# Optimization experiments

Measured on AMD Instinct MI355X. Metric: run time of the kernel, lower is better.

## Reference

```python
import jax, jax.numpy as jnp
import numpy as np

N, E = 50000, 800000
IN, HID, HEADS, OUT = 128, 64, 2, 32
SLOPE = 0.2  # PyG leaky_relu default


def gat_conv(x, edge_index, edge_attr, W, att_src, att_dst, W_edge, att_edge, bias,
             heads, out_ch, concat):
    n = x.shape[0]
    src, dst = edge_index[0], edge_index[1]
    # add_self_loops with fill_value='mean': self-loop attr = mean of incoming edge_attr
    ones = jnp.ones((src.shape[0],), x.dtype)
    deg = jax.ops.segment_sum(ones, dst, num_segments=n)
    loop_attr = jax.ops.segment_sum(edge_attr, dst, num_segments=n) / jnp.maximum(deg, 1.0)[:, None]
    ar = jnp.arange(n)
    src = jnp.concatenate([src, ar])
    dst = jnp.concatenate([dst, ar])
    ea = jnp.concatenate([edge_attr, loop_attr], axis=0)  # [E+N, 1]
    # linear projections
    h = (x @ W).reshape(n, heads, out_ch)                      # [N,H,C]
    a_src = jnp.sum(h * att_src, axis=-1)                      # [N,H]
    a_dst = jnp.sum(h * att_dst, axis=-1)                      # [N,H]
    e_emb = (ea @ W_edge).reshape(-1, heads, out_ch)           # [E+N,H,C]
    a_edge = jnp.sum(e_emb * att_edge, axis=-1)                # [E+N,H]
    alpha = jax.nn.leaky_relu(a_src[src] + a_dst[dst] + a_edge, SLOPE)
    # segment softmax over destination nodes
    amax = jax.ops.segment_max(alpha, dst, num_segments=n)
    amax = jnp.where(jnp.isfinite(amax), amax, 0.0)
    ex = jnp.exp(alpha - amax[dst])
    denom = jax.ops.segment_sum(ex, dst, num_segments=n)
    coef = ex / (denom[dst] + 1e-16)                           # [E+N,H]
    out = jax.ops.segment_sum(h[src] * coef[:, :, None], dst, num_segments=n)  # [N,H,C]
    out = out.reshape(n, heads * out_ch) if concat else out.mean(axis=1)
    return out + bias


def setup_inputs() -> dict:
    key = jax.random.key(0)
    ks = jax.random.split(key, 16)
    g = lambda k, shape, fan: (jax.random.normal(k, shape, jnp.float32) / np.float32(np.sqrt(fan)))
    x = jax.random.normal(ks[0], (N, IN), jnp.float32)
    edge_index = jax.random.randint(ks[1], (2, E), 0, N)
    edge_weight = jax.random.uniform(ks[2], (E, 1), jnp.float32)
    return dict(
        x=x, edge_index=edge_index, edge_weight=edge_weight,
        W1=g(ks[3], (IN, HEADS * HID), IN),
        att_src1=g(ks[4], (1, HEADS, HID), HID),
        att_dst1=g(ks[5], (1, HEADS, HID), HID),
        We1=g(ks[6], (1, HEADS * HID), 1),
        att_edge1=g(ks[7], (1, HEADS, HID), HID),
        b1=jnp.zeros((HEADS * HID,), jnp.float32),
        W2=g(ks[8], (HEADS * HID, OUT), HEADS * HID),
        att_src2=g(ks[9], (1, 1, OUT), OUT),
        att_dst2=g(ks[10], (1, 1, OUT), OUT),
        We2=g(ks[11], (1, OUT), 1),
        att_edge2=g(ks[12], (1, 1, OUT), OUT),
        b2=jnp.zeros((OUT,), jnp.float32),
    )


def reference(x, edge_index, edge_weight, W1, att_src1, att_dst1, We1, att_edge1, b1,
              W2, att_src2, att_dst2, We2, att_edge2, b2):
    h = gat_conv(x, edge_index, edge_weight, W1, att_src1, att_dst1, We1, att_edge1, b1,
                 HEADS, HID, True)
    h = jax.nn.elu(h)
    out = gat_conv(h, edge_index, edge_weight, W2, att_src2, att_dst2, We2, att_edge2, b2,
                   1, OUT, False)
    return out
```

## Files before the change

kernel.cpp:

```cpp
#include <hip/hip_runtime.h>
#include <hip/hip_bf16.h>
#include <hip/hip_fp16.h>
#include <cstddef>

#define NN 50000
#define EE 800000
#define SB  196

typedef _Float16 half4v __attribute__((ext_vector_type(4)));
typedef _Float16 half8v __attribute__((ext_vector_type(8)));
typedef _Float16 h2v    __attribute__((ext_vector_type(2)));
typedef float    f32x4  __attribute__((ext_vector_type(4)));

__global__ void zero_k(unsigned long long* __restrict__ p) {
    int i = blockIdx.x * blockDim.x + threadIdx.x;
    if (i < NN) p[i] = 0ULL;
}

__global__ void hist_k(const int* __restrict__ ei, const float* __restrict__ ew,
                       unsigned long long* __restrict__ packed, int* __restrict__ rank) {
    int e = blockIdx.x * blockDim.x + threadIdx.x;
    if (e >= EE) return;
    int dst = ei[EE + e];
    unsigned q = (unsigned)(ew[e] * 16777216.0f + 0.5f);
    unsigned long long old =
        atomicAdd(&packed[dst], (1ULL << 40) | (unsigned long long)q);
    rank[e] = (int)(old >> 40);
}

__global__ void loopdiv_k(const unsigned long long* __restrict__ packed,
                          int* __restrict__ deg, float* __restrict__ loopa,
                          int* __restrict__ bsum) {
    __shared__ int sm[256];
    int t = threadIdx.x, n = blockIdx.x * 256 + t;
    int d = 0;
    if (n < NN) {
        unsigned long long p = packed[n];
        d = (int)(p >> 40);
        float ls = (float)(p & ((1ULL << 40) - 1)) * (1.0f / 16777216.0f);
        deg[n] = d;
        loopa[n] = ls / fmaxf((float)d, 1.0f);
    }
    sm[t] = d;
    __syncthreads();
    for (int off = 128; off; off >>= 1) {
        if (t < off) sm[t] += sm[t + off];
        __syncthreads();
    }
    if (!t) bsum[blockIdx.x] = sm[0];
}

__global__ void scan_top_k(const int* __restrict__ bsum, int* __restrict__ boff) {
    __shared__ int sm[256];
    int t = threadIdx.x;
    int v = (t < SB) ? bsum[t] : 0;
    sm[t] = v;
    __syncthreads();
    for (int off = 1; off < 256; off <<= 1) {
        int a = (t >= off) ? sm[t - off] : 0;
        __syncthreads();
        sm[t] += a;
        __syncthreads();
    }
    boff[t] = sm[t] - v;
}

__global__ void scan_final_k(const int* __restrict__ deg, const int* __restrict__ boff,
                             int* __restrict__ rowptr) {
    __shared__ int sm[256];
    int t = threadIdx.x, i = blockIdx.x * 256 + t;
    int v = (i < NN) ? deg[i] : 0;
    sm[t] = v;
    __syncthreads();
    for (int off = 1; off < 256; off <<= 1) {
        int a = (t >= off) ? sm[t - off] : 0;
        __syncthreads();
        sm[t] += a;
        __syncthreads();
    }
    if (i < NN) rowptr[i] = boff[blockIdx.x] + sm[t] - v;
    if (i == NN - 1) rowptr[NN] = boff[blockIdx.x] + sm[t];
}

__global__ void scatter_k(const int* __restrict__ ei, const float* __restrict__ ew,
                          const int* __restrict__ rowptr, const int* __restrict__ rank,
                          int2* __restrict__ csr) {
    int e = blockIdx.x * blockDim.x + threadIdx.x;
    if (e >= EE) return;
    int src = ei[e];
    int dst = ei[EE + e];
    int pos = rowptr[dst] + rank[e];
    csr[pos] = make_int2(src, __float_as_int(ew[e]));
}

__global__ void consts_k(const float* __restrict__ We1, const float* __restrict__ attE1,
                         const float* __restrict__ We2, const float* __restrict__ attE2,
                         float* __restrict__ cE) {
    __shared__ float sm[128];
    int t = threadIdx.x;
    sm[t] = We1[t] * attE1[t];
    __syncthreads();
    for (int off = 32; off; off >>= 1) {
        if ((t & 63) < off) sm[t] += sm[t + off];
        __syncthreads();
    }
    if (t == 0)  cE[0] = sm[0];
    if (t == 64) cE[1] = sm[64];
    __syncthreads();
    sm[t] = (t < 32) ? We2[t] * attE2[t] : 0.0f;
    __syncthreads();
    for (int off = 16; off; off >>= 1) {
        if (t < off) sm[t] += sm[t + off];
        __syncthreads();
    }
    if (t == 0) cE[2] = sm[0];
}

__global__ __launch_bounds__(256) void gemm1_k(const float* __restrict__ x,
                                               const float* __restrict__ W,
                                               const float* __restrict__ attS,
                                               const float* __restrict__ attD,
                                               __half* __restrict__ h1,
                                               float* __restrict__ asrc,
                                               float* __restrict__ adst) {
    __shared__ __align__(16) _Float16 xs[64 * 136];
    int rowbase = blockIdx.x * 64;
    int t = threadIdx.x;
    int wid = t >> 6, lane = t & 63;
    #pragma unroll
    for (int i = 0; i < 8; i++) {
        int idx = t + i * 256;
        int r = idx >> 5;
        int c4 = idx & 31;
        float4 v = make_float4(0.f, 0.f, 0.f, 0.f);
        if (rowbase + r < NN) v = ((const float4*)x)[(size_t)(rowbase + r) * 32 + c4];
        half4v hv = { (_Float16)v.x, (_Float16)v.y, (_Float16)v.z, (_Float16)v.w };
        *(half4v*)&xs[r * 136 + c4 * 4] = hv;
    }
    half8v bf[2][4];
    #pragma unroll
    for (int nt = 0; nt < 2; nt++)
        #pragma unroll
        for (int kk = 0; kk < 4; kk++) {
            int kb = kk * 32 + ((lane >> 4) << 3);
            int c = (wid << 5) + (nt << 4) + (lane & 15);
            half8v f;
            #pragma unroll
            for (int j = 0; j < 8; j++) f[j] = (_Float16)W[(kb + j) * 128 + c];
            bf[nt][kk] = f;
        }
    __syncthreads();
    int ar = lane & 15;
    int ak = (lane >> 4) << 3;
    f32x4 acc[4][2] = {};
    #pragma unroll
    for (int kk = 0; kk < 4; kk++) {
        half8v a[4];
        #pragma unroll
        for (int mt = 0; mt < 4; mt++)
            a[mt] = *(const half8v*)&xs[(mt * 16 + ar) * 136 + kk * 32 + ak];
        #pragma unroll
        for (int mt = 0; mt < 4; mt++)
            #pragma unroll
            for (int nt = 0; nt < 2; nt++)
                acc[mt][nt] = __builtin_amdgcn_mfma_f32_16x16x32_f16(
                    a[mt], bf[nt][kk], acc[mt][nt], 0, 0, 0);
    }
    __syncthreads();
    int drb = (lane >> 4) << 2;
    int dc = (wid << 5) + (lane & 15);
    #pragma unroll
    for (int mt = 0; mt < 4; mt++)
        #pragma unroll
        for (int nt = 0; nt < 2; nt++)
            #pragma unroll
            for (int r = 0; r < 4; r++)
                xs[(mt * 16 + drb + r) * 136 + dc + nt * 16] = (_Float16)acc[mt][nt][r];
    __syncthreads();
    int row = t >> 2;
    int cg = t & 3;
    int grow = rowbase + row;
    float sv = 0.f, dv = 0.f;
    #pragma unroll
    for (int k = 0; k < 4; k++) {
        int c0 = cg * 32 + k * 8;
        half8v hv = *(const half8v*)&xs[row * 136 + c0];
        if (grow < NN) *(half8v*)((_Float16*)h1 + (size_t)grow * 128 + c0) = hv;
        #pragma unroll
        for (int j = 0; j < 8; j++) {
            float f = (float)hv[j];
            sv += f * attS[c0 + j];
            dv += f * attD[c0 + j];
        }
    }
    sv += __shfl_xor(sv, 1);
    dv += __shfl_xor(dv, 1);
    if ((cg & 1) == 0 && grow < NN) {
        asrc[grow * 2 + (cg >> 1)] = sv;
        adst[grow * 2 + (cg >> 1)] = dv;
    }
}

__global__ __launch_bounds__(256) void gemm2_k(const __half* __restrict__ z1,
                                               const float* __restrict__ W,
                                               const float* __restrict__ attS,
                                               const float* __restrict__ attD,
                                               __half* __restrict__ h2,
                                               float* __restrict__ asrc,
                                               float* __restrict__ adst) {
    __shared__ __align__(16) _Float16 xs[64 * 136];
    int rowbase = blockIdx.x * 64;
    int t = threadIdx.x;
    int wid = t >> 6, lane = t & 63;
    #pragma unroll
    for (int i = 0; i < 4; i++) {
        int idx = t + i * 256;
        int r = idx >> 4;
        int c16 = idx & 15;
        uint4 v = make_uint4(0, 0, 0, 0);
        if (rowbase + r < NN) v = ((const uint4*)z1)[(size_t)(rowbase + r) * 16 + c16];
        *(uint4*)&xs[r * 136 + c16 * 8] = v;
    }
    half8v bf[2][4];
    #pragma unroll
    for (int nt = 0; nt < 2; nt++)
        #pragma unroll
        for (int kk = 0; kk < 4; kk++) {
            int kb = kk * 32 + ((lane >> 4) << 3);
            int c = (nt << 4) + (lane & 15);
            half8v f;
            #pragma unroll
            for (int j = 0; j < 8; j++) f[j] = (_Float16)W[(kb + j) * 32 + c];
            bf[nt][kk] = f;
        }
    __syncthreads();
    int ar = lane & 15;
    int ak = (lane >> 4) << 3;
    f32x4 acc[2] = {};
    #pragma unroll
    for (int kk = 0; kk < 4; kk++) {
        half8v a = *(const half8v*)&xs[(wid * 16 + ar) * 136 + kk * 32 + ak];
        #pragma unroll
        for (int nt = 0; nt < 2; nt++)
            acc[nt] = __builtin_amdgcn_mfma_f32_16x16x32_f16(a, bf[nt][kk], acc[nt], 0, 0, 0);
    }
    __syncthreads();
    int drb = (lane >> 4) << 2;
    #pragma unroll
    for (int nt = 0; nt < 2; nt++)
        #pragma unroll
        for (int r = 0; r < 4; r++)
            xs[(wid * 16 + drb + r) * 40 + (nt << 4) + (lane & 15)] = (_Float16)acc[nt][r];
    __syncthreads();
    int row = t >> 2;
    int c8 = (t & 3) * 8;
    int grow = rowbase + row;
    half8v hv = *(const half8v*)&xs[row * 40 + c8];
    if (grow < NN) *(half8v*)((_Float16*)h2 + (size_t)grow * 32 + c8) = hv;
    float sv = 0.f, dv = 0.f;
    #pragma unroll
    for (int j = 0; j < 8; j++) {
        float f = (float)hv[j];
        sv += f * attS[c8 + j];
        dv += f * attD[c8 + j];
    }
    sv += __shfl_xor(sv, 1);
    dv += __shfl_xor(dv, 1);
    sv += __shfl_xor(sv, 2);
    dv += __shfl_xor(dv, 2);
    if ((t & 3) == 0 && grow < NN) { asrc[grow] = sv; adst[grow] = dv; }
}

__global__ __launch_bounds__(256) void agg1_k(const int* __restrict__ rowptr,
                       const int2* __restrict__ csr, const float* __restrict__ loopa,
                       const __half* __restrict__ h1, const float* __restrict__ asrc,
                       const float* __restrict__ adst, const float* __restrict__ cE,
                       const float* __restrict__ b1, __half* __restrict__ z1) {
    __shared__ int    ssrc[4][128];
    __shared__ float2 sxx[4][128];
    __shared__ int2   spk[4][136];
    int wid = threadIdx.x >> 6;
    int n = (blockIdx.x * blockDim.x + threadIdx.x) >> 6;
    int lane = threadIdx.x & 63;
    if (n >= NN) return;
    int start = rowptr[n];
    int degn = rowptr[n + 1] - start;
    int total = degn + 1;
    float c0 = cE[0], c1 = cE[1];
    float ad0 = adst[n * 2], ad1 = adst[n * 2 + 1];
    float la = loopa[n];
    float s0 = 0.f, s1 = 0.f;
    for (int i = lane; i < total; i += 64) {
        int src; float w;
        if (i < degn) { int2 sw = csr[start + i]; src = sw.x; w = __int_as_float(sw.y); }
        else          { src = n;                  w = la; }
        float2 as = *(const float2*)&asrc[src * 2];
        float e0 = as.x + ad0 + w * c0; e0 = e0 > 0.f ? e0 : 0.2f * e0;
        float e1 = as.y + ad1 + w * c1; e1 = e1 > 0.f ? e1 : 0.2f * e1;
        float x0 = __expf(e0), x1 = __expf(e1);
        s0 += x0; s1 += x1;
        if (i < 128) { ssrc[wid][i] = src; sxx[wid][i] = make_float2(x0, x1); }
    }
    for (int off = 32; off; off >>= 1) {
        s0 += __shfl_xor(s0, off);
        s1 += __shfl_xor(s1, off);
    }
    float inv0 = 1.0f / (s0 + 1e-16f), inv1 = 1.0f / (s1 + 1e-16f);
    int nst = min(total, 128);
    int nst8 = (nst + 7) & ~7;
    for (int i = lane; i < nst8; i += 64) {
        int2 pk;
        if (i < nst) {
            float2 xv = sxx[wid][i];
            __half2 hh = __floats2half2_rn(xv.x * inv0, xv.y * inv1);
            pk = make_int2(ssrc[wid][i], *(int*)&hh);
        } else pk = make_int2(n, 0);
        spk[wid][i] = pk;
    }
    int hsel = lane >> 5;
    unsigned psel = hsel ? 0x03020302u : 0x01000100u;
    unsigned loff = (unsigned)lane * 4u;
    const char* h1b_ = (const char*)h1;
    float acc0 = 0.f, acc1 = 0.f;
    for (int j = 0; j < nst8; j += 8) {
        h2v pa = {}, pb = {};
        #pragma unroll
        for (int u = 0; u < 8; u++) {
            int2 st = spk[wid][j + u];
            unsigned cs = __builtin_amdgcn_perm(0u, (unsigned)st.y, psel);
            unsigned hb = *(const unsigned*)(h1b_ + (((unsigned)st.x << 8) + loff));
            h2v c; __builtin_memcpy(&c, &cs, 4);
            h2v h; __builtin_memcpy(&h, &hb, 4);
            if (u & 1) pb = c * h + pb;
            else       pa = c * h + pa;
        }
        acc0 += (float)pa.x + (float)pb.x;
        acc1 += (float)pa.y + (float)pb.y;
    }
    for (int base = 128; base < total; base += 64) {
        int i = base + lane;
        float cc0 = 0.f, cc1 = 0.f; int src = n;
        if (i < total) {
            float w;
            if (i < degn) { int2 sw = csr[start + i]; src = sw.x; w = __int_as_float(sw.y); }
            else          { w = la; }
            float e0 = asrc[src * 2]     + ad0 + w * c0; e0 = e0 > 0.f ? e0 : 0.2f * e0;
            float e1 = asrc[src * 2 + 1] + ad1 + w * c1; e1 = e1 > 0.f ? e1 : 0.2f * e1;
            cc0 = __expf(e0) * inv0;
            cc1 = __expf(e1) * inv1;
        }
        int cnt = min(64, total - base);
        for (int jj = 0; jj < cnt; jj++) {
            int   s2 = __shfl(src, jj);
            float k0 = __shfl(cc0, jj);
            float k1 = __shfl(cc1, jj);
            float coef = hsel ? k1 : k0;
            float2 f = __half22float2(*(const __half2*)&h1[(size_t)s2 * 128 + 2 * lane]);
            acc0 += coef * f.x;
            acc1 += coef * f.y;
        }
    }
    float o0 = acc0 + b1[2 * lane];
    float o1 = acc1 + b1[2 * lane + 1];
    o0 = o0 > 0.f ? o0 : expm1f(o0);
    o1 = o1 > 0.f ? o1 : expm1f(o1);
    __half2 oz = __floats2half2_rn(o0, o1);
    *(__half2*)&z1[(size_t)n * 128 + 2 * lane] = oz;
}

__global__ __launch_bounds__(256) void agg2_k(const int* __restrict__ rowptr,
                       const int2* __restrict__ csr, const float* __restrict__ loopa,
                       const __half* __restrict__ hh2, const float* __restrict__ asrc,
                       const float* __restrict__ adst, const float* __restrict__ cE,
                       const float* __restrict__ b2, float* __restrict__ out) {
    __shared__ float2 sxx[4][128];
    __shared__ int    ssrc[4][128];
    __shared__ int2   spk[4][136];
    int wid = threadIdx.x >> 6;
    int n = (blockIdx.x * blockDim.x + threadIdx.x) >> 6;
    int lane = threadIdx.x & 63;
    if (n >= NN) return;
    int start = rowptr[n];
    int degn = rowptr[n + 1] - start;
    int total = degn + 1;
    float c2 = cE[2];
    float aD = adst[n];
    float la = loopa[n];
    float s = 0.f;
    for (int i = lane; i < total; i += 64) {
        int src; float w;
        if (i < degn) { int2 sw = csr[start + i]; src = sw.x; w = __int_as_float(sw.y); }
        else          { src = n;                  w = la; }
        float e = asrc[src] + aD + w * c2;
        e = e > 0.f ? e : 0.2f * e;
        float x = __expf(e);
        s += x;
        if (i < 128) { ssrc[wid][i] = src; sxx[wid][i] = make_float2(x, 0.f); }
    }
    for (int off = 32; off; off >>= 1) s += __shfl_xor(s, off);
    float inv = 1.0f / (s + 1e-16f);
    int nst = min(total, 128);
    int nst8 = (nst + 7) & ~7;
    for (int i = lane; i < nst8; i += 64) {
        int2 pk;
        if (i < nst) {
            float cn = sxx[wid][i].x * inv;
            __half2 hc = __floats2half2_rn(cn, cn);
            pk = make_int2(ssrc[wid][i], *(int*)&hc);
        } else pk = make_int2(n, 0);
        spk[wid][i] = pk;
    }
    int g  = lane >> 4;
    int cp = lane & 15;
    const char* h2b_ = (const char*)hh2;
    unsigned coff = (unsigned)cp * 4u;
    float fa0 = 0.f, fa1 = 0.f;
    h2v pa = {}, pb = {};
    int fold = 0;
    for (int j = 0; j < nst8; j += 8) {
        int2 st0 = spk[wid][j + g];
        int2 st1 = spk[wid][j + 4 + g];
        unsigned hb0 = *(const unsigned*)(h2b_ + (((unsigned)st0.x << 6) + coff));
        unsigned hb1 = *(const unsigned*)(h2b_ + (((unsigned)st1.x << 6) + coff));
        h2v c0v; __builtin_memcpy(&c0v, &st0.y, 4);
        h2v c1v; __builtin_memcpy(&c1v, &st1.y, 4);
        h2v h0; __builtin_memcpy(&h0, &hb0, 4);
        h2v h1v; __builtin_memcpy(&h1v, &hb1, 4);
        pa = c0v * h0 + pa;
        pb = c1v * h1v + pb;
        if (++fold == 4) {
            fa0 += (float)pa.x + (float)pb.x;
            fa1 += (float)pa.y + (float)pb.y;
            pa = {}; pb = {};
            fold = 0;
        }
    }
    fa0 += (float)pa.x + (float)pb.x;
    fa1 += (float)pa.y + (float)pb.y;
    for (int i = 128; i < total; i++) {
        int src; float w;
        if (i < degn) { int2 sw = csr[start + i]; src = sw.x; w = __int_as_float(sw.y); }
        else          { src = n;                  w = la; }
        float e = asrc[src] + aD + w * c2;
        e = e > 0.f ? e : 0.2f * e;
        float cc = __expf(e) * inv;
        if (g == 0) {
            unsigned hb = *(const unsigned*)(h2b_ + (((unsigned)src << 6) + coff));
            h2v h; __builtin_memcpy(&h, &hb, 4);
            fa0 += cc * (float)h.x;
            fa1 += cc * (float)h.y;
        }
    }
    fa0 += __shfl_xor(fa0, 16); fa1 += __shfl_xor(fa1, 16);
    fa0 += __shfl_xor(fa0, 32); fa1 += __shfl_xor(fa1, 32);
    if (lane < 16) {
        float2 o = make_float2(fa0 + b2[2 * cp], fa1 + b2[2 * cp + 1]);
        *(float2*)&out[(size_t)n * 32 + 2 * cp] = o;
    }
}

extern "C" void kernel_launch(void* const* d_in, const int* in_sizes, int n_in,
                              void* d_out, int out_size, void* d_ws, size_t ws_size,
                              hipStream_t stream) {
    const float* x     = (const float*)d_in[0];
    const int*   ei    = (const int*)d_in[1];
    const float* ew    = (const float*)d_in[2];
    const float* W1    = (const float*)d_in[3];
    const float* attS1 = (const float*)d_in[4];
    const float* attD1 = (const float*)d_in[5];
    const float* We1   = (const float*)d_in[6];
    const float* attE1 = (const float*)d_in[7];
    const float* b1    = (const float*)d_in[8];
    const float* W2    = (const float*)d_in[9];
    const float* attS2 = (const float*)d_in[10];
    const float* attD2 = (const float*)d_in[11];
    const float* We2   = (const float*)d_in[12];
    const float* attE2 = (const float*)d_in[13];
    const float* b2    = (const float*)d_in[14];

    char* ws = (char*)d_ws;
    size_t off = 0;
    auto alloc = [&](size_t bytes) -> void* {
        void* p = ws + off;
        off = (off + bytes + 255) & ~(size_t)255;
        return p;
    };
    unsigned long long* packed = (unsigned long long*)alloc((size_t)NN * 8);
    int*    rank    = (int*)alloc((size_t)EE * 4);
    int*    deg     = (int*)alloc((size_t)NN * 4);
    float*  loopa   = (float*)alloc((size_t)NN * 4);
    int*    rowptr  = (int*)alloc((size_t)(NN + 1) * 4);
    int2*   csr     = (int2*)alloc((size_t)EE * 8);
    __half* h1b     = (__half*)alloc((size_t)NN * 128 * 2);
    __half* z1      = (__half*)alloc((size_t)NN * 128 * 2);
    __half* h2b     = (__half*)alloc((size_t)NN * 32 * 2);
    float*  asrc1   = (float*)alloc((size_t)NN * 2 * 4);
    float*  adst1   = (float*)alloc((size_t)NN * 2 * 4);
    float*  asrc2   = (float*)alloc((size_t)NN * 4);
    float*  adst2   = (float*)alloc((size_t)NN * 4);
    float*  cE      = (float*)alloc(4 * 4);
    int*    bsum    = (int*)alloc(256 * 4);
    int*    boff    = (int*)alloc(256 * 4);

    const int EB  = (EE + 255) / 256;
    const int NWB = (NN * 64 + 255) / 256;
    const int GB  = (NN + 63) / 64;

    zero_k<<<SB, 256, 0, stream>>>(packed);
    hist_k<<<EB, 256, 0, stream>>>(ei, ew, packed, rank);
    consts_k<<<1, 128, 0, stream>>>(We1, attE1, We2, attE2, cE);
    loopdiv_k<<<SB, 256, 0, stream>>>(packed, deg, loopa, bsum);
    scan_top_k<<<1, 256, 0, stream>>>(bsum, boff);
    scan_final_k<<<SB, 256, 0, stream>>>(deg, boff, rowptr);
    scatter_k<<<EB, 256, 0, stream>>>(ei, ew, rowptr, rank, csr);

    gemm1_k<<<GB, 256, 0, stream>>>(x, W1, attS1, attD1, h1b, asrc1, adst1);
    agg1_k<<<NWB, 256, 0, stream>>>(rowptr, csr, loopa, h1b, asrc1, adst1, cE, b1, z1);

    gemm2_k<<<GB, 256, 0, stream>>>(z1, W2, attS2, attD2, h2b, asrc2, adst2);
    agg2_k<<<NWB, 256, 0, stream>>>(rowptr, csr, loopa, h2b, asrc2, adst2, cE, b2, (float*)d_out);
}
```

Measured before the change: 154.9 us.

## Merge small launches: fuse histogram with gemm1, consts into init, fold scan top

Folds the edge-weight constant reduction into the zeroing kernel, runs the degree histogram and the layer-1 GEMM as disjoint block ranges of a single launch, and has each final-scan block recompute its own prefix of block sums instead of using a separate top-level scan kernel. This cuts the launch count from eleven to eight and lets the independent histogram atomics overlap with the GEMM work. In exchange, histogram blocks now reserve the GEMM's shared memory, which may lower occupancy, and every scan block repeats a reduction over up to 196 block sums.

```diff
diff --git a/kernel.cpp b/kernel.cpp
--- a/kernel.cpp
+++ b/kernel.cpp
@@ -6,26 +6,136 @@
 #define NN 50000
 #define EE 800000
 #define SB  196
+#define EB  3125
+#define GB  782
 
 typedef _Float16 half4v __attribute__((ext_vector_type(4)));
 typedef _Float16 half8v __attribute__((ext_vector_type(8)));
 typedef _Float16 h2v    __attribute__((ext_vector_type(2)));
 typedef float    f32x4  __attribute__((ext_vector_type(4)));
 
-__global__ void zero_k(unsigned long long* __restrict__ p) {
-    int i = blockIdx.x * blockDim.x + threadIdx.x;
+__global__ void init_k(unsigned long long* __restrict__ p,
+                       const float* __restrict__ We1, const float* __restrict__ attE1,
+                       const float* __restrict__ We2, const float* __restrict__ attE2,
+                       float* __restrict__ cE) {
+    int t = threadIdx.x;
+    if (blockIdx.x == SB) {
+        __shared__ float smc[128];
+        if (t < 128) smc[t] = We1[t] * attE1[t];
+        __syncthreads();
+        for (int off = 32; off; off >>= 1) {
+            if (t < 128 && (t & 63) < off) smc[t] += smc[t + off];
+            __syncthreads();
+        }
+        if (t == 0)  cE[0] = smc[0];
+        if (t == 64) cE[1] = smc[64];
+        __syncthreads();
+        if (t < 32) smc[t] = We2[t] * attE2[t];
+        __syncthreads();
+        for (int off = 16; off; off >>= 1) {
+            if (t < off) smc[t] += smc[t + off];
+            __syncthreads();
+        }
+        if (t == 0) cE[2] = smc[0];
+        return;
+    }
+    int i = blockIdx.x * blockDim.x + t;
     if (i < NN) p[i] = 0ULL;
 }
 
-__global__ void hist_k(const int* __restrict__ ei, const float* __restrict__ ew,
-                       unsigned long long* __restrict__ packed, int* __restrict__ rank) {
-    int e = blockIdx.x * blockDim.x + threadIdx.x;
-    if (e >= EE) return;
-    int dst = ei[EE + e];
-    unsigned q = (unsigned)(ew[e] * 16777216.0f + 0.5f);
-    unsigned long long old =
-        atomicAdd(&packed[dst], (1ULL << 40) | (unsigned long long)q);
-    rank[e] = (int)(old >> 40);
+__global__ __launch_bounds__(256) void hist_gemm1_k(
+        const int* __restrict__ ei, const float* __restrict__ ew,
+        unsigned long long* __restrict__ packed, int* __restrict__ rank,
+        const float* __restrict__ x, const float* __restrict__ W,
+        const float* __restrict__ attS, const float* __restrict__ attD,
+        __half* __restrict__ h1, float* __restrict__ asrc, float* __restrict__ adst) {
+    __shared__ __align__(16) _Float16 xs[64 * 136];
+    int t = threadIdx.x;
+    if (blockIdx.x < EB) {
+        int e = blockIdx.x * 256 + t;
+        if (e < EE) {
+            int dst = ei[EE + e];
+            unsigned q = (unsigned)(ew[e] * 16777216.0f + 0.5f);
+            unsigned long long old =
+                atomicAdd(&packed[dst], (1ULL << 40) | (unsigned long long)q);
+            rank[e] = (int)(old >> 40);
+        }
+        return;
+    }
+    int rowbase = (blockIdx.x - EB) * 64;
+    int wid = t >> 6, lane = t & 63;
+    #pragma unroll
+    for (int i = 0; i < 8; i++) {
+        int idx = t + i * 256;
+        int r = idx >> 5;
+        int c4 = idx & 31;
+        float4 v = make_float4(0.f, 0.f, 0.f, 0.f);
+        if (rowbase + r < NN) v = ((const float4*)x)[(size_t)(rowbase + r) * 32 + c4];
+        half4v hv = { (_Float16)v.x, (_Float16)v.y, (_Float16)v.z, (_Float16)v.w };
+        *(half4v*)&xs[r * 136 + c4 * 4] = hv;
+    }
+    half8v bf[2][4];
+    #pragma unroll
+    for (int nt = 0; nt < 2; nt++)
+        #pragma unroll
+        for (int kk = 0; kk < 4; kk++) {
+            int kb = kk * 32 + ((lane >> 4) << 3);
+            int c = (wid << 5) + (nt << 4) + (lane & 15);
+            half8v f;
+            #pragma unroll
+            for (int j = 0; j < 8; j++) f[j] = (_Float16)W[(kb + j) * 128 + c];
+            bf[nt][kk] = f;
+        }
+    __syncthreads();
+    int ar = lane & 15;
+    int ak = (lane >> 4) << 3;
+    f32x4 acc[4][2] = {};
+    #pragma unroll
+    for (int kk = 0; kk < 4; kk++) {
+        half8v a[4];
+        #pragma unroll
+        for (int mt = 0; mt < 4; mt++)
+            a[mt] = *(const half8v*)&xs[(mt * 16 + ar) * 136 + kk * 32 + ak];
+        #pragma unroll
+        for (int mt = 0; mt < 4; mt++)
+            #pragma unroll
+            for (int nt = 0; nt < 2; nt++)
+                acc[mt][nt] = __builtin_amdgcn_mfma_f32_16x16x32_f16(
+                    a[mt], bf[nt][kk], acc[mt][nt], 0, 0, 0);
+    }
+    __syncthreads();
+    int drb = (lane >> 4) << 2;
+    int dc = (wid << 5) + (lane & 15);
+    #pragma unroll
+    for (int mt = 0; mt < 4; mt++)
+        #pragma unroll
+        for (int nt = 0; nt < 2; nt++)
+            #pragma unroll
+            for (int r = 0; r < 4; r++)
+                xs[(mt * 16 + drb + r) * 136 + dc + nt * 16] = (_Float16)acc[mt][nt][r];
+    __syncthreads();
+    int row = t >> 2;
+    int cg = t & 3;
+    int grow = rowbase + row;
+    float sv = 0.f, dv = 0.f;
+    #pragma unroll
+    for (int k = 0; k < 4; k++) {
+        int c0 = cg * 32 + k * 8;
+        half8v hv = *(const half8v*)&xs[row * 136 + c0];
+        if (grow < NN) *(half8v*)((_Float16*)h1 + (size_t)grow * 128 + c0) = hv;
+        #pragma unroll
+        for (int j = 0; j < 8; j++) {
+            float f = (float)hv[j];
+            sv += f * attS[c0 + j];
+            dv += f * attD[c0 + j];
+        }
+    }
+    sv += __shfl_xor(sv, 1);
+    dv += __shfl_xor(dv, 1);
+    if ((cg & 1) == 0 && grow < NN) {
+        asrc[grow * 2 + (cg >> 1)] = sv;
+        adst[grow * 2 + (cg >> 1)] = dv;
+    }
 }
 
 __global__ void loopdiv_k(const unsigned long long* __restrict__ packed,
@@ -50,10 +160,21 @@
     if (!t) bsum[blockIdx.x] = sm[0];
 }
 
-__global__ void scan_top_k(const int* __restrict__ bsum, int* __restrict__ boff) {
+__global__ void scan_final_k(const int* __restrict__ deg, const int* __restrict__ bsum,
+                             int* __restrict__ rowptr) {
     __shared__ int sm[256];
-    int t = threadIdx.x;
-    int v = (t < SB) ? bsum[t] : 0;
+    __shared__ int boff_s;
+    int t = threadIdx.x, b = blockIdx.x, i = b * 256 + t;
+    int v0 = (t < b) ? bsum[t] : 0;
+    sm[t] = v0;
+    __syncthreads();
+    for (int off = 128; off; off >>= 1) {
+        if (t < off) sm[t] += sm[t + off];
+        __syncthreads();
+    }
+    if (!t) boff_s = sm[0];
+    __syncthreads();
+    int v = (i < NN) ? deg[i] : 0;
     sm[t] = v;
     __syncthreads();
     for (int off = 1; off < 256; off <<= 1) {
@@ -62,24 +183,8 @@
         sm[t] += a;
         __syncthreads();
     }
-    boff[t] = sm[t] - v;
-}
-
-__global__ void scan_final_k(const int* __restrict__ deg, const int* __restrict__ boff,
-                             int* __restrict__ rowptr) {
-    __shared__ int sm[256];
-    int t = threadIdx.x, i = blockIdx.x * 256 + t;
-    int v = (i < NN) ? deg[i] : 0;
-    sm[t] = v;
-    __syncthreads();
-    for (int off = 1; off < 256; off <<= 1) {
-        int a = (t >= off) ? sm[t - off] : 0;
-        __syncthreads();
-        sm[t] += a;
-        __syncthreads();
-    }
-    if (i < NN) rowptr[i] = boff[blockIdx.x] + sm[t] - v;
-    if (i == NN - 1) rowptr[NN] = boff[blockIdx.x] + sm[t];
+    if (i < NN) rowptr[i] = boff_s + sm[t] - v;
+    if (i == NN - 1) rowptr[NN] = boff_s + sm[t];
 }
 
 __global__ void scatter_k(const int* __restrict__ ei, const float* __restrict__ ew,
@@ -91,114 +196,6 @@
     int dst = ei[EE + e];
     int pos = rowptr[dst] + rank[e];
     csr[pos] = make_int2(src, __float_as_int(ew[e]));
-}
-
-__global__ void consts_k(const float* __restrict__ We1, const float* __restrict__ attE1,
-                         const float* __restrict__ We2, const float* __restrict__ attE2,
-                         float* __restrict__ cE) {
-    __shared__ float sm[128];
-    int t = threadIdx.x;
-    sm[t] = We1[t] * attE1[t];
-    __syncthreads();
-    for (int off = 32; off; off >>= 1) {
-        if ((t & 63) < off) sm[t] += sm[t + off];
-        __syncthreads();
-    }
-    if (t == 0)  cE[0] = sm[0];
-    if (t == 64) cE[1] = sm[64];
-    __syncthreads();
-    sm[t] = (t < 32) ? We2[t] * attE2[t] : 0.0f;
-    __syncthreads();
-    for (int off = 16; off; off >>= 1) {
-        if (t < off) sm[t] += sm[t + off];
-        __syncthreads();
-    }
-    if (t == 0) cE[2] = sm[0];
-}
-
-__global__ __launch_bounds__(256) void gemm1_k(const float* __restrict__ x,
-                                               const float* __restrict__ W,
-                                               const float* __restrict__ attS,
-                                               const float* __restrict__ attD,
-                                               __half* __restrict__ h1,
-                                               float* __restrict__ asrc,
-                                               float* __restrict__ adst) {
-    __shared__ __align__(16) _Float16 xs[64 * 136];
-    int rowbase = blockIdx.x * 64;
-    int t = threadIdx.x;
-    int wid = t >> 6, lane = t & 63;
-    #pragma unroll
-    for (int i = 0; i < 8; i++) {
-        int idx = t + i * 256;
-        int r = idx >> 5;
-        int c4 = idx & 31;
-        float4 v = make_float4(0.f, 0.f, 0.f, 0.f);
-        if (rowbase + r < NN) v = ((const float4*)x)[(size_t)(rowbase + r) * 32 + c4];
-        half4v hv = { (_Float16)v.x, (_Float16)v.y, (_Float16)v.z, (_Float16)v.w };
-        *(half4v*)&xs[r * 136 + c4 * 4] = hv;
-    }
-    half8v bf[2][4];
-    #pragma unroll
-    for (int nt = 0; nt < 2; nt++)
-        #pragma unroll
-        for (int kk = 0; kk < 4; kk++) {
-            int kb = kk * 32 + ((lane >> 4) << 3);
-            int c = (wid << 5) + (nt << 4) + (lane & 15);
-            half8v f;
-            #pragma unroll
-            for (int j = 0; j < 8; j++) f[j] = (_Float16)W[(kb + j) * 128 + c];
-            bf[nt][kk] = f;
-        }
-    __syncthreads();
-    int ar = lane & 15;
-    int ak = (lane >> 4) << 3;
-    f32x4 acc[4][2] = {};
-    #pragma unroll
-    for (int kk = 0; kk < 4; kk++) {
-        half8v a[4];
-        #pragma unroll
-        for (int mt = 0; mt < 4; mt++)
-            a[mt] = *(const half8v*)&xs[(mt * 16 + ar) * 136 + kk * 32 + ak];
-        #pragma unroll
-        for (int mt = 0; mt < 4; mt++)
-            #pragma unroll
-            for (int nt = 0; nt < 2; nt++)
-                acc[mt][nt] = __builtin_amdgcn_mfma_f32_16x16x32_f16(
-                    a[mt], bf[nt][kk], acc[mt][nt], 0, 0, 0);
-    }
-    __syncthreads();
-    int drb = (lane >> 4) << 2;
-    int dc = (wid << 5) + (lane & 15);
-    #pragma unroll
-    for (int mt = 0; mt < 4; mt++)
-        #pragma unroll
-        for (int nt = 0; nt < 2; nt++)
-            #pragma unroll
-            for (int r = 0; r < 4; r++)
-                xs[(mt * 16 + drb + r) * 136 + dc + nt * 16] = (_Float16)acc[mt][nt][r];
-    __syncthreads();
-    int row = t >> 2;
-    int cg = t & 3;
-    int grow = rowbase + row;
-    float sv = 0.f, dv = 0.f;
-    #pragma unroll
-    for (int k = 0; k < 4; k++) {
-        int c0 = cg * 32 + k * 8;
-        half8v hv = *(const half8v*)&xs[row * 136 + c0];
-        if (grow < NN) *(half8v*)((_Float16*)h1 + (size_t)grow * 128 + c0) = hv;
-        #pragma unroll
-        for (int j = 0; j < 8; j++) {
-            float f = (float)hv[j];
-            sv += f * attS[c0 + j];
-            dv += f * attD[c0 + j];
-        }
-    }
-    sv += __shfl_xor(sv, 1);
-    dv += __shfl_xor(dv, 1);
-    if ((cg & 1) == 0 && grow < NN) {
-        asrc[grow * 2 + (cg >> 1)] = sv;
-        adst[grow * 2 + (cg >> 1)] = dv;
-    }
 }
 
 __global__ __launch_bounds__(256) void gemm2_k(const __half* __restrict__ z1,
@@ -500,23 +497,17 @@
     float*  adst2   = (float*)alloc((size_t)NN * 4);
     float*  cE      = (float*)alloc(4 * 4);
     int*    bsum    = (int*)alloc(256 * 4);
-    int*    boff    = (int*)alloc(256 * 4);
-
-    const int EB  = (EE + 255) / 256;
+
     const int NWB = (NN * 64 + 255) / 256;
-    const int GB  = (NN + 63) / 64;
-
-    zero_k<<<SB, 256, 0, stream>>>(packed);
-    hist_k<<<EB, 256, 0, stream>>>(ei, ew, packed, rank);
-    consts_k<<<1, 128, 0, stream>>>(We1, attE1, We2, attE2, cE);
+
+    init_k<<<SB + 1, 256, 0, stream>>>(packed, We1, attE1, We2, attE2, cE);
+    hist_gemm1_k<<<EB + GB, 256, 0, stream>>>(ei, ew, packed, rank,
+                                              x, W1, attS1, attD1, h1b, asrc1, adst1);
     loopdiv_k<<<SB, 256, 0, stream>>>(packed, deg, loopa, bsum);
-    scan_top_k<<<1, 256, 0, stream>>>(bsum, boff);
-    scan_final_k<<<SB, 256, 0, stream>>>(deg, boff, rowptr);
+    scan_final_k<<<SB, 256, 0, stream>>>(deg, bsum, rowptr);
     scatter_k<<<EB, 256, 0, stream>>>(ei, ew, rowptr, rank, csr);
 
-    gemm1_k<<<GB, 256, 0, stream>>>(x, W1, attS1, attD1, h1b, asrc1, adst1);
     agg1_k<<<NWB, 256, 0, stream>>>(rowptr, csr, loopa, h1b, asrc1, adst1, cE, b1, z1);
-
     gemm2_k<<<GB, 256, 0, stream>>>(z1, W2, attS2, attD2, h2b, asrc2, adst2);
     agg2_k<<<NWB, 256, 0, stream>>>(rowptr, csr, loopa, h2b, asrc2, adst2, cE, b2, (float*)d_out);
 }
```

After: 147.8 us. -4.6%, faster.
